# Kernel optimization log

Measured on AMD Instinct MI355X. Metric: run time of the kernel, lower is better.

The kernel has to match this reference:

```python
import jax, jax.numpy as jnp
import numpy as np
import math

N_HEAD = 16
N_CTX = 1024


def setup_inputs() -> dict:
    key = jax.random.key(0)
    ks = jax.random.split(key, 3)
    B, S, NX = 4, 1024, 1024
    x = jax.random.normal(ks[0], (B, S, NX), dtype=jnp.float32)
    # Conv1D weights stored as [nx, nf], init std=0.02, bias zeros
    c_attn_w = jax.random.normal(ks[1], (NX, 3 * NX), dtype=jnp.float32) * 0.02
    c_attn_b = jnp.zeros((3 * NX,), dtype=jnp.float32)
    c_proj_w = jax.random.normal(ks[2], (NX, NX), dtype=jnp.float32) * 0.02
    c_proj_b = jnp.zeros((NX,), dtype=jnp.float32)
    return {"x": x, "c_attn_w": c_attn_w, "c_attn_b": c_attn_b,
            "c_proj_w": c_proj_w, "c_proj_b": c_proj_b}


def reference(x, c_attn_w, c_attn_b, c_proj_w, c_proj_b):
    B, S, NX = x.shape
    H = N_HEAD
    D = NX // H
    # c_attn: Conv1D -> x @ W + b, then split into q, k, v
    qkv = x @ c_attn_w + c_attn_b                      # [B,S,3*NX]
    q, k, v = jnp.split(qkv, 3, axis=-1)               # each [B,S,NX]
    # split heads: q,v -> [B,H,S,D]; k -> [B,H,D,S]
    q = q.reshape(B, S, H, D).transpose(0, 2, 1, 3)
    k = k.reshape(B, S, H, D).transpose(0, 2, 3, 1)
    v = v.reshape(B, S, H, D).transpose(0, 2, 1, 3)
    # _attn: scores, scale, combined multiplicative+additive causal mask, softmax
    w = jnp.matmul(q, k)                               # [B,H,S,S]
    w = w / math.sqrt(D)                               # scale=True
    bias = jnp.tril(jnp.ones((S, S), dtype=w.dtype))[None, None]  # causal tril slice
    w = w * bias - 1e10 * (1.0 - bias)
    w = jax.nn.softmax(w, axis=-1)
    a = jnp.matmul(w, v)                               # [B,H,S,D]
    # merge heads
    a = a.transpose(0, 2, 1, 3).reshape(B, S, NX)
    # c_proj
    return a @ c_proj_w + c_proj_b
```

## Files before the change

### kernel.cpp

```cpp
#include <hip/hip_runtime.h>
#include <cstdint>

typedef __attribute__((ext_vector_type(8))) short short8;
typedef __attribute__((ext_vector_type(4))) short short4x;
typedef __attribute__((ext_vector_type(4))) float floatx4;

__device__ __forceinline__ unsigned short f2b(float f) {
    unsigned int u = __builtin_bit_cast(unsigned int, f);
    u += 0x7fffu + ((u >> 16) & 1u);
    return (unsigned short)(u >> 16);
}
__device__ __forceinline__ float b2f(unsigned short s) {
    unsigned int u = ((unsigned int)s) << 16;
    return __builtin_bit_cast(float, u);
}

#define GLDS(g, l) __builtin_amdgcn_global_load_lds(                                   \
    (const __attribute__((address_space(1))) unsigned int*)(g),                        \
    (__attribute__((address_space(3))) unsigned int*)(l), 16, 0, 0)

__global__ __launch_bounds__(256) void cvt_bf16_kernel(const float* __restrict__ in,
                                                       unsigned short* __restrict__ out, int n4) {
    int i = blockIdx.x * blockDim.x + threadIdx.x;
    if (i >= n4) return;
    float4 v = ((const float4*)in)[i];
    ushort4 o;
    o.x = f2b(v.x); o.y = f2b(v.y); o.z = f2b(v.z); o.w = f2b(v.w);
    ((ushort4*)out)[i] = o;
}

__global__ __launch_bounds__(256) void transpose_cvt_kernel(const float* __restrict__ W,
                                                            unsigned short* __restrict__ Wt,
                                                            int K, int N) {
    __shared__ unsigned short tile[64][65];
    int k0 = blockIdx.x * 64, n0 = blockIdx.y * 64;
    for (int idx = threadIdx.x; idx < 64 * 64; idx += 256) {
        int i = idx >> 6, j = idx & 63;
        tile[j][i] = f2b(W[(size_t)(k0 + i) * N + n0 + j]);
    }
    __syncthreads();
    for (int idx = threadIdx.x; idx < 64 * 64; idx += 256) {
        int r = idx >> 6, c = idx & 63;
        Wt[(size_t)(n0 + r) * K + k0 + c] = tile[r][c];
    }
}

__global__ __launch_bounds__(256) void vtrans_kernel(const unsigned short* __restrict__ qkv,
                                                     unsigned short* __restrict__ vT) {
    __shared__ unsigned short tile[64][65];
    const int st = blockIdx.x * 64;
    const int bh = blockIdx.y;
    const int b = bh >> 4, h = bh & 15;
    const int t = threadIdx.x;
#pragma unroll
    for (int p = 0; p < 2; ++p) {
        int c = t + p * 256;
        int srow = c >> 3, dcol = (c & 7) * 8;
        short8 v = *(const short8*)(qkv + (size_t)(b * 1024 + st + srow) * 3072 + 2048 + h * 64 + dcol);
#pragma unroll
        for (int e = 0; e < 8; ++e) tile[dcol + e][srow] = (unsigned short)v[e];
    }
    __syncthreads();
#pragma unroll
    for (int p = 0; p < 2; ++p) {
        int c = t + p * 256;
        int drow = c >> 3, scol = (c & 7) * 8;
        short8 v;
#pragma unroll
        for (int e = 0; e < 8; ++e) v[e] = (short)tile[drow][scol + e];
        *(short8*)(vT + ((size_t)bh * 64 + drow) * 1024 + st + scol) = v;
    }
}

template <int OUT_BF16>
__global__ __launch_bounds__(256) void gemm_bt_kernel(const unsigned short* __restrict__ A,
                                                      const unsigned short* __restrict__ Bt,
                                                      const float* __restrict__ bias,
                                                      void* __restrict__ Cv,
                                                      int M, int N, int K) {
    __shared__ unsigned short As[128][32];
    __shared__ unsigned short Bs[128][32];

    const int t = threadIdx.x;
    const int wave = t >> 6, lane = t & 63;
    const int quad = lane >> 4, l16 = lane & 15;
    const int rowBase = blockIdx.x * 128;
    const int colBase = blockIdx.y * 128;
    const int waveM = (wave >> 1) * 64;
    const int waveN = (wave & 1) * 64;

    floatx4 acc[4][4];
#pragma unroll
    for (int i = 0; i < 4; ++i)
#pragma unroll
        for (int j = 0; j < 4; ++j) acc[i][j] = (floatx4){0.f, 0.f, 0.f, 0.f};

    const int c0 = t, c1 = t + 256;
    const int r0 = c0 >> 2, cc0 = (c0 & 3) * 8;
    const int r1 = c1 >> 2, cc1 = (c1 & 3) * 8;

    const unsigned short* aBase = A + (size_t)rowBase * K;
    const unsigned short* bBase = Bt + (size_t)colBase * K;

    for (int k0 = 0; k0 < K; k0 += 32) {
        GLDS(aBase + (size_t)r0 * K + k0 + cc0, &As[r0][cc0]);
        GLDS(aBase + (size_t)r1 * K + k0 + cc1, &As[r1][cc1]);
        GLDS(bBase + (size_t)r0 * K + k0 + cc0, &Bs[r0][cc0]);
        GLDS(bBase + (size_t)r1 * K + k0 + cc1, &Bs[r1][cc1]);
        __syncthreads();

        short8 af[4], bf[4];
#pragma unroll
        for (int mi = 0; mi < 4; ++mi)
            af[mi] = *(const short8*)&As[waveM + mi * 16 + l16][quad * 8];
#pragma unroll
        for (int ni = 0; ni < 4; ++ni)
            bf[ni] = *(const short8*)&Bs[waveN + ni * 16 + l16][quad * 8];
#pragma unroll
        for (int mi = 0; mi < 4; ++mi)
#pragma unroll
            for (int ni = 0; ni < 4; ++ni)
                acc[mi][ni] = __builtin_amdgcn_mfma_f32_16x16x32_bf16(af[mi], bf[ni], acc[mi][ni], 0, 0, 0);
        __syncthreads();
    }

#pragma unroll
    for (int mi = 0; mi < 4; ++mi)
#pragma unroll
        for (int ni = 0; ni < 4; ++ni) {
            int col = colBase + waveN + ni * 16 + l16;
            float bv = bias[col];
#pragma unroll
            for (int r = 0; r < 4; ++r) {
                int row = rowBase + waveM + mi * 16 + quad * 4 + r;
                float v = acc[mi][ni][r] + bv;
                if (OUT_BF16)
                    ((unsigned short*)Cv)[(size_t)row * N + col] = f2b(v);
                else
                    ((float*)Cv)[(size_t)row * N + col] = v;
            }
        }
}

__global__ __launch_bounds__(256) void attn_kernel(const unsigned short* __restrict__ qkv,
                                                   const unsigned short* __restrict__ vT,
                                                   unsigned short* __restrict__ aout) {
    __shared__ unsigned short Ks[2 * 64 * 64];
    __shared__ unsigned short Vs[2 * 64 * 64];
    __shared__ unsigned short Tb[4][16 * 72];

    const int p  = blockIdx.x;
    const int bh = blockIdx.y;
    const int b = bh >> 4, h = bh & 15;
    const int qb1 = p, qb2 = 15 - p;
    const int t = threadIdx.x;
    const int wave = t >> 6, lane = t & 63;
    const int quad = lane >> 4, l16 = lane & 15;
    const int h7 = l16 & 7;

    const size_t rowB = (size_t)b * 1024;
    const size_t hoff = (size_t)h * 64;
    const int qA0 = qb1 * 64 + wave * 16;
    const int qB0 = qb2 * 64 + wave * 16;

    short8 qfA[2], qfB[2];
#pragma unroll
    for (int kc = 0; kc < 2; ++kc) {
        short8 qa = *(const short8*)(qkv + (rowB + qA0 + l16) * 3072 + hoff + kc * 32 + quad * 8);
        short8 qb = *(const short8*)(qkv + (rowB + qB0 + l16) * 3072 + hoff + kc * 32 + quad * 8);
#pragma unroll
        for (int e = 0; e < 8; ++e) {
            qa[e] = (short)f2b(b2f((unsigned short)qa[e]) * 0.125f);
            qb[e] = (short)f2b(b2f((unsigned short)qb[e]) * 0.125f);
        }
        qfA[kc] = qa; qfB[kc] = qb;
    }

    const int lr = lane >> 3;
    const int sc8 = (lane & 7) * 8;
    const int gc8 = ((lane & 7) ^ lr) * 8;
    const unsigned short* kSrc = qkv + rowB * 3072 + hoff + 1024;
    const unsigned short* vSrc = vT + (size_t)bh * 65536;

    auto stage = [&](int kt, int bf) {
        const unsigned short* kp = kSrc + (size_t)kt * 64 * 3072;
        const unsigned short* vp = vSrc + kt * 64;
        int r0 = wave * 16 + lr, r1 = r0 + 8;
        GLDS(kp + (size_t)r0 * 3072 + gc8, &Ks[bf * 4096 + r0 * 64 + sc8]);
        GLDS(kp + (size_t)r1 * 3072 + gc8, &Ks[bf * 4096 + r1 * 64 + sc8]);
        GLDS(vp + (size_t)r0 * 1024 + gc8, &Vs[bf * 4096 + r0 * 64 + sc8]);
        GLDS(vp + (size_t)r1 * 1024 + gc8, &Vs[bf * 4096 + r1 * 64 + sc8]);
    };

    float lpA = 0.f, lpB = 0.f;
    floatx4 oA[4], oB[4];
#pragma unroll
    for (int ni = 0; ni < 4; ++ni) {
        oA[ni] = (floatx4){0.f, 0.f, 0.f, 0.f};
        oB[ni] = (floatx4){0.f, 0.f, 0.f, 0.f};
    }

    const int nT = qb2 + 1;
    stage(0, 0);

    for (int kt = 0; kt < nT; ++kt) {
        __syncthreads();
        if (kt + 1 < nT) stage(kt + 1, (kt + 1) & 1);
        const int kb = (kt & 1) * 4096;

        short8 kf[4][2];
#pragma unroll
        for (int jn = 0; jn < 4; ++jn)
#pragma unroll
            for (int kc = 0; kc < 2; ++kc)
                kf[jn][kc] = *(const short8*)&Ks[kb + (jn * 16 + l16) * 64 + (((kc * 4 + quad) ^ h7) * 8)];

        short4x vf[4][4];
#pragma unroll
        for (int ni = 0; ni < 4; ++ni)
#pragma unroll
            for (int jb = 0; jb < 4; ++jb)
                vf[ni][jb] = *(const short4x*)&Vs[kb + (ni * 16 + l16) * 64 +
                                                 (((jb * 2 + (quad >> 1)) ^ h7) * 8) + (quad & 1) * 4];

        auto qtile = [&](short8 (&qf)[2], floatx4 (&o)[4], float& lp, bool diag) {
            floatx4 s[4];
#pragma unroll
            for (int jn = 0; jn < 4; ++jn) s[jn] = (floatx4){0.f, 0.f, 0.f, 0.f};
#pragma unroll
            for (int jn = 0; jn < 4; ++jn)
#pragma unroll
                for (int kc = 0; kc < 2; ++kc)
                    s[jn] = __builtin_amdgcn_mfma_f32_16x16x32_bf16(kf[jn][kc], qf[kc], s[jn], 0, 0, 0);
            if (diag) {
                int ql = wave * 16 + l16;
#pragma unroll
                for (int jn = 0; jn < 4; ++jn)
#pragma unroll
                    for (int r = 0; r < 4; ++r)
                        if (jn * 16 + quad * 4 + r > ql) s[jn][r] = -1e30f;
            }
            short4x pb[4];
#pragma unroll
            for (int jb = 0; jb < 4; ++jb)
#pragma unroll
                for (int r = 0; r < 4; ++r) {
                    float pe = __expf(s[jb][r]);
                    lp += pe;
                    pb[jb][r] = (short)f2b(pe);
                }
#pragma unroll
            for (int jb = 0; jb < 4; ++jb)
#pragma unroll
                for (int ni = 0; ni < 4; ++ni)
                    o[ni] = __builtin_amdgcn_mfma_f32_16x16x16bf16_1k(vf[ni][jb], pb[jb], o[ni], 0, 0, 0);
        };

        qtile(qfB, oB, lpB, kt == qb2);
        if (kt <= qb1) qtile(qfA, oA, lpA, kt == qb1);
    }

    lpA += __shfl_xor(lpA, 16); lpA += __shfl_xor(lpA, 32);
    lpB += __shfl_xor(lpB, 16); lpB += __shfl_xor(lpB, 32);
    const float liA = 1.f / lpA, liB = 1.f / lpB;

    auto writeOut = [&](floatx4 (&o)[4], float li, int q0) {
#pragma unroll
        for (int ni = 0; ni < 4; ++ni)
#pragma unroll
            for (int r = 0; r < 4; ++r)
                Tb[wave][l16 * 72 + ni * 16 + quad * 4 + r] = f2b(o[ni][r] * li);
#pragma unroll
        for (int i = 0; i < 2; ++i) {
            int q = lane >> 2, c = (lane & 3) + 4 * i;
            short8 v = *(const short8*)&Tb[wave][q * 72 + c * 8];
            *(short8*)(aout + (rowB + q0 + q) * 1024 + hoff + c * 8) = v;
        }
    };
    writeOut(oA, liA, qA0);
    writeOut(oB, liB, qB0);
}

extern "C" void kernel_launch(void* const* d_in, const int* in_sizes, int n_in,
                              void* d_out, int out_size, void* d_ws, size_t ws_size,
                              hipStream_t stream) {
    const float* x  = (const float*)d_in[0];
    const float* w1 = (const float*)d_in[1];
    const float* b1 = (const float*)d_in[2];
    const float* w2 = (const float*)d_in[3];
    const float* b2 = (const float*)d_in[4];
    float* out = (float*)d_out;

    unsigned short* xb   = (unsigned short*)d_ws;
    unsigned short* w1t  = xb  + (size_t)4096 * 1024;
    unsigned short* w2t  = w1t + (size_t)3072 * 1024;
    unsigned short* qkv  = w2t + (size_t)1024 * 1024;
    unsigned short* attn = qkv + (size_t)4096 * 3072;
    unsigned short* vTb  = attn + (size_t)4096 * 1024;

    cvt_bf16_kernel<<<4096, 256, 0, stream>>>(x, xb, 4096 * 1024 / 4);
    transpose_cvt_kernel<<<dim3(16, 48), 256, 0, stream>>>(w1, w1t, 1024, 3072);
    transpose_cvt_kernel<<<dim3(16, 16), 256, 0, stream>>>(w2, w2t, 1024, 1024);

    gemm_bt_kernel<1><<<dim3(32, 24), 256, 0, stream>>>(xb, w1t, b1, qkv, 4096, 3072, 1024);
    vtrans_kernel<<<dim3(16, 64), 256, 0, stream>>>(qkv, vTb);
    attn_kernel<<<dim3(8, 64), 256, 0, stream>>>(qkv, vTb, attn);
    gemm_bt_kernel<0><<<dim3(32, 8), 256, 0, stream>>>(attn, w2t, b2, out, 4096, 1024, 1024);
}
```

Baseline: 183.4 us.

## Fuse V transpose into QKV GEMM epilogue and stage outputs through LDS

Removes the separate V-transpose kernel. The QKV GEMM now writes the V column blocks directly in transposed [b,h,d,s] layout by staging the tile in shared memory. All GEMM epilogues also stage their tiles through LDS so global stores are coalesced 16-byte vectors instead of scattered scalar stores. This saves one kernel launch and a read/write pass over V, at the cost of extra LDS traffic, barriers and a larger shared-memory footprint, which may reduce occupancy.

```diff
diff --git a/kernel.cpp b/kernel.cpp
--- a/kernel.cpp
+++ b/kernel.cpp
@@ -45,41 +45,17 @@
     }
 }
 
-__global__ __launch_bounds__(256) void vtrans_kernel(const unsigned short* __restrict__ qkv,
-                                                     unsigned short* __restrict__ vT) {
-    __shared__ unsigned short tile[64][65];
-    const int st = blockIdx.x * 64;
-    const int bh = blockIdx.y;
-    const int b = bh >> 4, h = bh & 15;
-    const int t = threadIdx.x;
-#pragma unroll
-    for (int p = 0; p < 2; ++p) {
-        int c = t + p * 256;
-        int srow = c >> 3, dcol = (c & 7) * 8;
-        short8 v = *(const short8*)(qkv + (size_t)(b * 1024 + st + srow) * 3072 + 2048 + h * 64 + dcol);
-#pragma unroll
-        for (int e = 0; e < 8; ++e) tile[dcol + e][srow] = (unsigned short)v[e];
-    }
-    __syncthreads();
-#pragma unroll
-    for (int p = 0; p < 2; ++p) {
-        int c = t + p * 256;
-        int drow = c >> 3, scol = (c & 7) * 8;
-        short8 v;
-#pragma unroll
-        for (int e = 0; e < 8; ++e) v[e] = (short)tile[drow][scol + e];
-        *(short8*)(vT + ((size_t)bh * 64 + drow) * 1024 + st + scol) = v;
-    }
-}
-
 template <int OUT_BF16>
 __global__ __launch_bounds__(256) void gemm_bt_kernel(const unsigned short* __restrict__ A,
                                                       const unsigned short* __restrict__ Bt,
                                                       const float* __restrict__ bias,
                                                       void* __restrict__ Cv,
+                                                      unsigned short* __restrict__ vTout,
+                                                      int vSplit,
                                                       int M, int N, int K) {
-    __shared__ unsigned short As[128][32];
-    __shared__ unsigned short Bs[128][32];
+    __shared__ __align__(16) unsigned char smem_raw[34816];
+    unsigned short (*As)[32] = (unsigned short(*)[32])smem_raw;
+    unsigned short (*Bs)[32] = (unsigned short(*)[32])(smem_raw + 8192);
 
     const int t = threadIdx.x;
     const int wave = t >> 6, lane = t & 63;
@@ -124,22 +100,78 @@
         __syncthreads();
     }
 
-#pragma unroll
-    for (int mi = 0; mi < 4; ++mi)
+    if (OUT_BF16 && colBase >= vSplit) {
+        unsigned short (*Ct)[136] = (unsigned short(*)[136])smem_raw;
 #pragma unroll
         for (int ni = 0; ni < 4; ++ni) {
-            int col = colBase + waveN + ni * 16 + l16;
-            float bv = bias[col];
-#pragma unroll
-            for (int r = 0; r < 4; ++r) {
-                int row = rowBase + waveM + mi * 16 + quad * 4 + r;
-                float v = acc[mi][ni][r] + bv;
-                if (OUT_BF16)
-                    ((unsigned short*)Cv)[(size_t)row * N + col] = f2b(v);
-                else
-                    ((float*)Cv)[(size_t)row * N + col] = v;
+            int c = waveN + ni * 16 + l16;
+            float bv = bias[colBase + c];
+#pragma unroll
+            for (int mi = 0; mi < 4; ++mi)
+#pragma unroll
+                for (int r = 0; r < 4; ++r)
+                    Ct[c][waveM + mi * 16 + quad * 4 + r] = f2b(acc[mi][ni][r] + bv);
+        }
+        __syncthreads();
+        const int b = rowBase >> 10, s0 = rowBase & 1023;
+        const int vcol0 = colBase - vSplit;
+#pragma unroll
+        for (int p = 0; p < 8; ++p) {
+            int idx = t + p * 256;
+            int c = idx >> 4, ch = idx & 15;
+            int hh = (vcol0 + c) >> 6, d = c & 63;
+            short8 v = *(const short8*)&Ct[c][ch * 8];
+            *(short8*)(vTout + ((size_t)(b * 16 + hh) * 64 + d) * 1024 + s0 + ch * 8) = v;
+        }
+    } else if (OUT_BF16) {
+        unsigned short (*Cs)[136] = (unsigned short(*)[136])smem_raw;
+#pragma unroll
+        for (int ni = 0; ni < 4; ++ni) {
+            int c = waveN + ni * 16 + l16;
+            float bv = bias[colBase + c];
+#pragma unroll
+            for (int mi = 0; mi < 4; ++mi)
+#pragma unroll
+                for (int r = 0; r < 4; ++r)
+                    Cs[waveM + mi * 16 + quad * 4 + r][c] = f2b(acc[mi][ni][r] + bv);
+        }
+        __syncthreads();
+        unsigned short* C = (unsigned short*)Cv;
+#pragma unroll
+        for (int p = 0; p < 8; ++p) {
+            int idx = t + p * 256;
+            int row = idx >> 4, ch = idx & 15;
+            short8 v = *(const short8*)&Cs[row][ch * 8];
+            *(short8*)(C + (size_t)(rowBase + row) * N + colBase + ch * 8) = v;
+        }
+    } else {
+        float (*Cf)[132] = (float(*)[132])smem_raw;
+        float* C = (float*)Cv;
+#pragma unroll
+        for (int half = 0; half < 2; ++half) {
+            __syncthreads();
+            if ((wave >> 1) == half) {
+#pragma unroll
+                for (int ni = 0; ni < 4; ++ni) {
+                    int c = waveN + ni * 16 + l16;
+                    float bv = bias[colBase + c];
+#pragma unroll
+                    for (int mi = 0; mi < 4; ++mi)
+#pragma unroll
+                        for (int r = 0; r < 4; ++r)
+                            Cf[mi * 16 + quad * 4 + r][c] = acc[mi][ni][r] + bv;
+                }
             }
-        }
+            __syncthreads();
+#pragma unroll
+            for (int p = 0; p < 8; ++p) {
+                int idx = t + p * 256;
+                int row = idx >> 5, ch = idx & 31;
+                float4 v = *(const float4*)&Cf[row][ch * 4];
+                *(float4*)(C + (size_t)(rowBase + half * 64 + row) * N + colBase + ch * 4) = v;
+            }
+        }
+    }
 }
 
 __global__ __launch_bounds__(256) void attn_kernel(const unsigned short* __restrict__ qkv,
@@ -302,8 +334,9 @@
     transpose_cvt_kernel<<<dim3(16, 48), 256, 0, stream>>>(w1, w1t, 1024, 3072);
     transpose_cvt_kernel<<<dim3(16, 16), 256, 0, stream>>>(w2, w2t, 1024, 1024);
 
-    gemm_bt_kernel<1><<<dim3(32, 24), 256, 0, stream>>>(xb, w1t, b1, qkv, 4096, 3072, 1024);
-    vtrans_kernel<<<dim3(16, 64), 256, 0, stream>>>(qkv, vTb);
+    gemm_bt_kernel<1><<<dim3(32, 24), 256, 0, stream>>>(xb, w1t, b1, qkv, vTb, 2048,
+                                                        4096, 3072, 1024);
     attn_kernel<<<dim3(8, 64), 256, 0, stream>>>(qkv, vTb, attn);
-    gemm_bt_kernel<0><<<dim3(32, 8), 256, 0, stream>>>(attn, w2t, b2, out, 4096, 1024, 1024);
-}
+    gemm_bt_kernel<0><<<dim3(32, 8), 256, 0, stream>>>(attn, w2t, b2, out, nullptr, 1 << 30,
+                                                       4096, 1024, 1024);
+}
```

Measured after the change: 194.1 us. +5.8%, slower.

## Double-buffer GEMM LDS tiles, merge prep kernels, retile output projection

Applied to the files above, without the earlier changes.

The separate input-conversion and weight-transpose launches are folded into one prep kernel that dispatches on block index. The bf16-output QKV GEMM now uses two LDS buffers and issues the next tile's global-to-LDS loads right after the barrier, so those loads overlap the MFMA work and one barrier per iteration is dropped. The output projection moves to a new 64x64-tile kernel, giving four times as many blocks to fill the CUs, at the cost of less data reuse per block.

```diff
diff --git a/kernel.cpp b/kernel.cpp
--- a/kernel.cpp
+++ b/kernel.cpp
@@ -19,27 +19,33 @@
     (const __attribute__((address_space(1))) unsigned int*)(g),                        \
     (__attribute__((address_space(3))) unsigned int*)(l), 16, 0, 0)
 
-__global__ __launch_bounds__(256) void cvt_bf16_kernel(const float* __restrict__ in,
-                                                       unsigned short* __restrict__ out, int n4) {
-    int i = blockIdx.x * blockDim.x + threadIdx.x;
-    if (i >= n4) return;
-    float4 v = ((const float4*)in)[i];
-    ushort4 o;
-    o.x = f2b(v.x); o.y = f2b(v.y); o.z = f2b(v.z); o.w = f2b(v.w);
-    ((ushort4*)out)[i] = o;
-}
-
-__global__ __launch_bounds__(256) void transpose_cvt_kernel(const float* __restrict__ W,
-                                                            unsigned short* __restrict__ Wt,
-                                                            int K, int N) {
+__global__ __launch_bounds__(256) void prep_kernel(const float* __restrict__ x,
+                                                   unsigned short* __restrict__ xb,
+                                                   const float* __restrict__ w1,
+                                                   unsigned short* __restrict__ w1t,
+                                                   const float* __restrict__ w2,
+                                                   unsigned short* __restrict__ w2t) {
     __shared__ unsigned short tile[64][65];
-    int k0 = blockIdx.x * 64, n0 = blockIdx.y * 64;
-    for (int idx = threadIdx.x; idx < 64 * 64; idx += 256) {
+    const int b = blockIdx.x, t = threadIdx.x;
+    if (b < 1024) {
+        for (int i = b * 256 + t; i < 1048576; i += 262144) {
+            float4 v = ((const float4*)x)[i];
+            ushort4 o;
+            o.x = f2b(v.x); o.y = f2b(v.y); o.z = f2b(v.z); o.w = f2b(v.w);
+            ((ushort4*)xb)[i] = o;
+        }
+        return;
+    }
+    const float* W; unsigned short* Wt; int K, N, kb, nb;
+    if (b < 1792) { W = w1; Wt = w1t; K = 1024; N = 3072; kb = (b - 1024) & 15; nb = (b - 1024) >> 4; }
+    else          { W = w2; Wt = w2t; K = 1024; N = 1024; kb = (b - 1792) & 15; nb = (b - 1792) >> 4; }
+    const int k0 = kb * 64, n0 = nb * 64;
+    for (int idx = t; idx < 64 * 64; idx += 256) {
         int i = idx >> 6, j = idx & 63;
         tile[j][i] = f2b(W[(size_t)(k0 + i) * N + n0 + j]);
     }
     __syncthreads();
-    for (int idx = threadIdx.x; idx < 64 * 64; idx += 256) {
+    for (int idx = t; idx < 64 * 64; idx += 256) {
         int r = idx >> 6, c = idx & 63;
         Wt[(size_t)(n0 + r) * K + k0 + c] = tile[r][c];
     }
@@ -72,14 +78,13 @@
     }
 }
 
-template <int OUT_BF16>
 __global__ __launch_bounds__(256) void gemm_bt_kernel(const unsigned short* __restrict__ A,
                                                       const unsigned short* __restrict__ Bt,
                                                       const float* __restrict__ bias,
-                                                      void* __restrict__ Cv,
+                                                      unsigned short* __restrict__ C,
                                                       int M, int N, int K) {
-    __shared__ unsigned short As[128][32];
-    __shared__ unsigned short Bs[128][32];
+    __shared__ unsigned short As[2][128][32];
+    __shared__ unsigned short Bs[2][128][32];
 
     const int t = threadIdx.x;
     const int wave = t >> 6, lane = t & 63;
@@ -95,33 +100,39 @@
 #pragma unroll
         for (int j = 0; j < 4; ++j) acc[i][j] = (floatx4){0.f, 0.f, 0.f, 0.f};
 
-    const int c0 = t, c1 = t + 256;
-    const int r0 = c0 >> 2, cc0 = (c0 & 3) * 8;
-    const int r1 = c1 >> 2, cc1 = (c1 & 3) * 8;
-
+    const int r0 = t >> 2, cc0 = (t & 3) * 8;
+    const int r1 = 64 + (t >> 2);
     const unsigned short* aBase = A + (size_t)rowBase * K;
     const unsigned short* bBase = Bt + (size_t)colBase * K;
 
-    for (int k0 = 0; k0 < K; k0 += 32) {
-        GLDS(aBase + (size_t)r0 * K + k0 + cc0, &As[r0][cc0]);
-        GLDS(aBase + (size_t)r1 * K + k0 + cc1, &As[r1][cc1]);
-        GLDS(bBase + (size_t)r0 * K + k0 + cc0, &Bs[r0][cc0]);
-        GLDS(bBase + (size_t)r1 * K + k0 + cc1, &Bs[r1][cc1]);
+    auto stage = [&](int kk, int bf) {
+        const int k0 = kk * 32;
+        GLDS(aBase + (size_t)r0 * K + k0 + cc0, &As[bf][r0][cc0]);
+        GLDS(aBase + (size_t)r1 * K + k0 + cc0, &As[bf][r1][cc0]);
+        GLDS(bBase + (size_t)r0 * K + k0 + cc0, &Bs[bf][r0][cc0]);
+        GLDS(bBase + (size_t)r1 * K + k0 + cc0, &Bs[bf][r1][cc0]);
+    };
+
+    const int nIter = K >> 5;
+    stage(0, 0);
+
+    for (int kk = 0; kk < nIter; ++kk) {
         __syncthreads();
+        if (kk + 1 < nIter) stage(kk + 1, (kk + 1) & 1);
+        const int buf = kk & 1;
 
         short8 af[4], bf[4];
 #pragma unroll
         for (int mi = 0; mi < 4; ++mi)
-            af[mi] = *(const short8*)&As[waveM + mi * 16 + l16][quad * 8];
+            af[mi] = *(const short8*)&As[buf][waveM + mi * 16 + l16][quad * 8];
 #pragma unroll
         for (int ni = 0; ni < 4; ++ni)
-            bf[ni] = *(const short8*)&Bs[waveN + ni * 16 + l16][quad * 8];
+            bf[ni] = *(const short8*)&Bs[buf][waveN + ni * 16 + l16][quad * 8];
 #pragma unroll
         for (int mi = 0; mi < 4; ++mi)
 #pragma unroll
             for (int ni = 0; ni < 4; ++ni)
                 acc[mi][ni] = __builtin_amdgcn_mfma_f32_16x16x32_bf16(af[mi], bf[ni], acc[mi][ni], 0, 0, 0);
-        __syncthreads();
     }
 
 #pragma unroll
@@ -133,11 +144,75 @@
 #pragma unroll
             for (int r = 0; r < 4; ++r) {
                 int row = rowBase + waveM + mi * 16 + quad * 4 + r;
-                float v = acc[mi][ni][r] + bv;
-                if (OUT_BF16)
-                    ((unsigned short*)Cv)[(size_t)row * N + col] = f2b(v);
-                else
-                    ((float*)Cv)[(size_t)row * N + col] = v;
+                C[(size_t)row * N + col] = f2b(acc[mi][ni][r] + bv);
+            }
+        }
+}
+
+__global__ __launch_bounds__(256) void gemm2_kernel(const unsigned short* __restrict__ A,
+                                                    const unsigned short* __restrict__ Bt,
+                                                    const float* __restrict__ bias,
+                                                    float* __restrict__ C,
+                                                    int M, int N, int K) {
+    __shared__ unsigned short As[2][64][32];
+    __shared__ unsigned short Bs[2][64][32];
+
+    const int t = threadIdx.x;
+    const int wave = t >> 6, lane = t & 63;
+    const int quad = lane >> 4, l16 = lane & 15;
+    const int rowBase = blockIdx.x * 64;
+    const int colBase = blockIdx.y * 64;
+    const int waveM = (wave >> 1) * 32;
+    const int waveN = (wave & 1) * 32;
+
+    floatx4 acc[2][2];
+#pragma unroll
+    for (int i = 0; i < 2; ++i)
+#pragma unroll
+        for (int j = 0; j < 2; ++j) acc[i][j] = (floatx4){0.f, 0.f, 0.f, 0.f};
+
+    const int r0 = t >> 2, cc0 = (t & 3) * 8;
+    const unsigned short* aBase = A + (size_t)rowBase * K;
+    const unsigned short* bBase = Bt + (size_t)colBase * K;
+
+    auto stage = [&](int kk, int bf) {
+        const int k0 = kk * 32;
+        GLDS(aBase + (size_t)r0 * K + k0 + cc0, &As[bf][r0][cc0]);
+        GLDS(bBase + (size_t)r0 * K + k0 + cc0, &Bs[bf][r0][cc0]);
+    };
+
+    const int nIter = K >> 5;
+    stage(0, 0);
+
+    for (int kk = 0; kk < nIter; ++kk) {
+        __syncthreads();
+        if (kk + 1 < nIter) stage(kk + 1, (kk + 1) & 1);
+        const int buf = kk & 1;
+
+        short8 af[2], bf[2];
+#pragma unroll
+        for (int mi = 0; mi < 2; ++mi)
+            af[mi] = *(const short8*)&As[buf][waveM + mi * 16 + l16][quad * 8];
+#pragma unroll
+        for (int ni = 0; ni < 2; ++ni)
+            bf[ni] = *(const short8*)&Bs[buf][waveN + ni * 16 + l16][quad * 8];
+#pragma unroll
+        for (int mi = 0; mi < 2; ++mi)
+#pragma unroll
+            for (int ni = 0; ni < 2; ++ni)
+                acc[mi][ni] = __builtin_amdgcn_mfma_f32_16x16x32_bf16(af[mi], bf[ni], acc[mi][ni], 0, 0, 0);
+    }
+
+#pragma unroll
+    for (int mi = 0; mi < 2; ++mi)
+#pragma unroll
+        for (int ni = 0; ni < 2; ++ni) {
+            int col = colBase + waveN + ni * 16 + l16;
+            float bv = bias[col];
+#pragma unroll
+            for (int r = 0; r < 4; ++r) {
+                int row = rowBase + waveM + mi * 16 + quad * 4 + r;
+                C[(size_t)row * N + col] = acc[mi][ni][r] + bv;
             }
         }
 }
@@ -298,12 +373,9 @@
     unsigned short* attn = qkv + (size_t)4096 * 3072;
     unsigned short* vTb  = attn + (size_t)4096 * 1024;
 
-    cvt_bf16_kernel<<<4096, 256, 0, stream>>>(x, xb, 4096 * 1024 / 4);
-    transpose_cvt_kernel<<<dim3(16, 48), 256, 0, stream>>>(w1, w1t, 1024, 3072);
-    transpose_cvt_kernel<<<dim3(16, 16), 256, 0, stream>>>(w2, w2t, 1024, 1024);
-
-    gemm_bt_kernel<1><<<dim3(32, 24), 256, 0, stream>>>(xb, w1t, b1, qkv, 4096, 3072, 1024);
+    prep_kernel<<<2048, 256, 0, stream>>>(x, xb, w1, w1t, w2, w2t);
+    gemm_bt_kernel<<<dim3(32, 24), 256, 0, stream>>>(xb, w1t, b1, qkv, 4096, 3072, 1024);
     vtrans_kernel<<<dim3(16, 64), 256, 0, stream>>>(qkv, vTb);
     attn_kernel<<<dim3(8, 64), 256, 0, stream>>>(qkv, vTb, attn);
-    gemm_bt_kernel<0><<<dim3(32, 8), 256, 0, stream>>>(attn, w2t, b2, out, 4096, 1024, 1024);
-}
+    gemm2_kernel<<<dim3(64, 16), 256, 0, stream>>>(attn, w2t, b2, out, 4096, 1024, 1024);
+}
```

Result: faster. 166.3 us (-9.3%).
